# Optimization experiments

Measured on AMD Instinct MI355X. Metric: run time of the kernel, lower is better.

Reference implementation:

```python
import jax, jax.numpy as jnp
import numpy as np

N = 50000       # num nodes
F_IN = 256      # num_features
HID = 128       # num_hidden
E = 800000      # structural edges (no self loops)
E_KNN = 500000  # knn edges (no self loops)


def setup_inputs() -> dict:
    rng = np.random.default_rng(0)
    # loop-free random edges: col != row guaranteed
    row = rng.integers(0, N, E)
    col = (row + 1 + rng.integers(0, N - 1, E)) % N
    edge_index = jnp.asarray(np.stack([row, col]), dtype=jnp.int32)
    rowk = rng.integers(0, N, E_KNN)
    colk = (rowk + 1 + rng.integers(0, N - 1, E_KNN)) % N
    knn_graph = jnp.asarray(np.stack([rowk, colk]), dtype=jnp.int32)

    key = jax.random.key(0)
    ks = jax.random.split(key, 8)
    x = jax.random.normal(ks[0], (N, F_IN), dtype=jnp.float32)
    s = 1.0 / np.sqrt(F_IN)  # nn.Linear default init range
    def lin(kw, kb):
        W = jax.random.uniform(kw, (HID, F_IN), minval=-s, maxval=s, dtype=jnp.float32)
        b = jax.random.uniform(kb, (HID,), minval=-s, maxval=s, dtype=jnp.float32)
        return W, b
    W_s1, b_s1 = lin(ks[1], ks[2])
    W_s2, b_s2 = lin(ks[3], ks[4])
    W_f2, b_f2 = lin(ks[5], ks[6])
    return {"x": x, "edge_index": edge_index, "knn_graph": knn_graph,
            "W_s1": W_s1, "b_s1": b_s1, "W_s2": W_s2, "b_s2": b_s2,
            "W_f2": W_f2, "b_f2": b_f2}


def _gcn_norm(edge_index, num_nodes):
    # add_remaining_self_loops on loop-free input == append all self loops (w=1)
    loop = jnp.arange(num_nodes, dtype=edge_index.dtype)
    row = jnp.concatenate([edge_index[0], loop])
    col = jnp.concatenate([edge_index[1], loop])
    w = jnp.ones(row.shape[0], dtype=jnp.float32)
    deg = jax.ops.segment_sum(w, col, num_segments=num_nodes)
    dinv = jnp.where(deg > 0, jax.lax.rsqrt(deg), 0.0)
    return row, col, dinv[row] * w * dinv[col]


def _gcn(x, W, b, row, col, norm, K):
    # eval mode: dropout(p=0.6) is identity
    h = x @ W.T + b
    n = x.shape[0]
    for _ in range(K):
        # gather source feats -> edge-weight scale -> scatter-add to targets (SpMM)
        h = jax.ops.segment_sum(norm[:, None] * h[row], col, num_segments=n)
    return h


def reference(x, edge_index, knn_graph, W_s1, b_s1, W_s2, b_s2, W_f2, b_f2):
    n = x.shape[0]
    r, c, nm = _gcn_norm(edge_index, n)
    rk, ck, nmk = _gcn_norm(knn_graph, n)
    h0 = _gcn(x, W_s1, b_s1, r, c, nm, 2)
    h1 = _gcn(x, W_s2, b_s2, r, c, nm, 10)
    z0 = _gcn(x, W_f2, b_f2, r, c, nm, 2)
    # original computes gcn_f2(x, edge_index, K=2) twice; in eval mode both equal z0
    z1 = z0 + _gcn(x, W_f2, b_f2, rk, ck, nmk, 1)
    return (h0, h1, z0, z1)
```

## Files before the change

### kernel.cpp

```cpp
#include <hip/hip_runtime.h>
#include <hip/hip_fp16.h>

#define F_IN 256
#define HID 128

typedef _Float16 half8 __attribute__((ext_vector_type(8)));
typedef _Float16 half4v __attribute__((ext_vector_type(4)));
typedef float f32x4 __attribute__((ext_vector_type(4)));


__global__ void k_count(const int* __restrict__ col, int E, int* __restrict__ cnt) {
  int e = blockIdx.x * blockDim.x + threadIdx.x;
  if (e < E) atomicAdd(&cnt[col[e]], 1);
}

__global__ void k_scan_block(const int* __restrict__ in, int n, int* __restrict__ out,
                             int* __restrict__ bsum) {
  __shared__ int s[1024];
  int tid = threadIdx.x;
  int i = blockIdx.x * 1024 + tid;
  int v = (i < n) ? in[i] : 0;
  s[tid] = v;
  __syncthreads();
  for (int off = 1; off < 1024; off <<= 1) {
    int t = (tid >= off) ? s[tid - off] : 0;
    __syncthreads();
    s[tid] += t;
    __syncthreads();
  }
  if (i < n) out[i] = s[tid] - v;
  if (tid == 1023) bsum[blockIdx.x] = s[1023];
}

__global__ void k_scan_single(int* __restrict__ bsum, int nb, int* __restrict__ tail) {
  if (threadIdx.x == 0 && blockIdx.x == 0) {
    int run = 0;
    for (int b = 0; b < nb; ++b) { int t = bsum[b]; bsum[b] = run; run += t; }
    *tail = run;
  }
}

__global__ void k_add_off(int* __restrict__ out, const int* __restrict__ bsum, int n) {
  int i = blockIdx.x * blockDim.x + threadIdx.x;
  if (i < n) out[i] += bsum[i >> 10];
}

__global__ void k_scatter(const int* __restrict__ row, const int* __restrict__ col, int E,
                          const int* __restrict__ offs, int* __restrict__ cur,
                          int* __restrict__ csr) {
  int e = blockIdx.x * blockDim.x + threadIdx.x;
  if (e >= E) return;
  int c = col[e];
  int p = offs[c] + atomicAdd(&cur[c], 1);
  csr[p] = row[e];
}


__global__ void k_cvt_w(const float* __restrict__ W0, const float* __restrict__ W1,
                        const float* __restrict__ W2, _Float16* __restrict__ Wh) {
  const int sz = HID * F_IN;
  int idx = (blockIdx.x * 256 + threadIdx.x) * 4;
  const float* src = (idx < sz) ? (W0 + idx)
                   : (idx < 2 * sz) ? (W1 + idx - sz)
                   : (W2 + idx - 2 * sz);
  float4 v = *(const float4*)src;
  half4v o;
  o[0] = (_Float16)v.x; o[1] = (_Float16)v.y; o[2] = (_Float16)v.z; o[3] = (_Float16)v.w;
  *(half4v*)(Wh + idx) = o;
}


__global__ __launch_bounds__(256) void k_gemm3(
    const float* __restrict__ x, const _Float16* __restrict__ Wh,
    const float* __restrict__ b0, const float* __restrict__ b1, const float* __restrict__ b2,
    int n, const int* __restrict__ cnt_s, const int* __restrict__ cnt_k,
    _Float16* __restrict__ gS1, _Float16* __restrict__ gS2,
    _Float16* __restrict__ gF2s, _Float16* __restrict__ gF2k)
{
  int lane = threadIdx.x & 63;
  int wv = threadIdx.x >> 6;
  int l15 = lane & 15, lhi = lane >> 4;
  int mrow = blockIdx.x * 64 + wv * 16 + l15;
  bool mok = mrow < n;

  half8 a[8];
  {
    const float* xr = x + (size_t)mrow * F_IN;
#pragma unroll
    for (int kt = 0; kt < 8; ++kt) {
      float4 lo = make_float4(0.f, 0.f, 0.f, 0.f), hi = lo;
      if (mok) {
        lo = *(const float4*)(xr + kt * 32 + lhi * 8);
        hi = *(const float4*)(xr + kt * 32 + lhi * 8 + 4);
      }
      half8 v;
      v[0] = (_Float16)lo.x; v[1] = (_Float16)lo.y; v[2] = (_Float16)lo.z; v[3] = (_Float16)lo.w;
      v[4] = (_Float16)hi.x; v[5] = (_Float16)hi.y; v[6] = (_Float16)hi.z; v[7] = (_Float16)hi.w;
      a[kt] = v;
    }
  }

  float ss = 1.0f, sk = 1.0f;
  if (mok) {
    ss = rsqrtf((float)(cnt_s[mrow] + 1));
    sk = rsqrtf((float)(cnt_k[mrow] + 1));
  }

#pragma unroll
  for (int w = 0; w < 3; ++w) {
    const _Float16* Wp = Wh + (size_t)w * HID * F_IN;
    const float* bias = (w == 0) ? b0 : (w == 1) ? b1 : b2;
    _Float16* dst = (w == 0) ? gS1 : (w == 1) ? gS2 : gF2s;
    for (int nt = 0; nt < 8; ++nt) {
      const _Float16* wrow = Wp + (size_t)(nt * 16 + l15) * F_IN;
      int nbase = nt * 16 + lhi * 4;
      float4 bv = *(const float4*)(bias + nbase);
      f32x4 acc = {bv.x, bv.y, bv.z, bv.w};
#pragma unroll
      for (int kt = 0; kt < 8; ++kt) {
        half8 bf = *(const half8*)(wrow + kt * 32 + lhi * 8);
        acc = __builtin_amdgcn_mfma_f32_16x16x32_f16(bf, a[kt], acc, 0, 0, 0);
      }
      if (mok) {
        half4v o;
        o[0] = (_Float16)(acc[0] * ss); o[1] = (_Float16)(acc[1] * ss);
        o[2] = (_Float16)(acc[2] * ss); o[3] = (_Float16)(acc[3] * ss);
        *(half4v*)(dst + (size_t)mrow * HID + nbase) = o;
        if (w == 2) {
          half4v o2;
          o2[0] = (_Float16)(acc[0] * sk); o2[1] = (_Float16)(acc[1] * sk);
          o2[2] = (_Float16)(acc[2] * sk); o2[3] = (_Float16)(acc[3] * sk);
          *(half4v*)(gF2k + (size_t)mrow * HID + nbase) = o2;
        }
      }
    }
  }
}


__device__ inline float2 h2f2(unsigned int u) {
  __half2 h; *(unsigned int*)&h = u; return __half22float2(h);
}

__device__ inline void spmm_store(void* out, size_t base, float2 acc, float deg, int mode,
                                  const float2* __restrict__ add) {
  if (mode == 0) {
    float sc = 1.0f / deg;
    __half2 h = __float22half2_rn(make_float2(acc.x * sc, acc.y * sc));
    ((__half2*)out)[base] = h;
  } else {
    float sc = rsqrtf(deg);
    float2 o = make_float2(acc.x * sc, acc.y * sc);
    if (mode == 2) { float2 z = add[base]; o.x += z.x; o.y += z.y; }
    ((float2*)out)[base] = o;
  }
}

__global__ __launch_bounds__(256) void k_spmm_h(
    const unsigned int* __restrict__ gin, void* __restrict__ gout,
    const int* __restrict__ csr, const int* __restrict__ offs, const int* __restrict__ cnt,
    int n, int mode, const float2* __restrict__ addsrc)
{
  int w = (blockIdx.x << 2) | ((int)threadIdx.x >> 6);
  if (w >= n) return;
  int lane = threadIdx.x & 63;
  int beg = offs[w], end = offs[w + 1];
  size_t base = (size_t)w * 64 + lane;
  float2 acc = h2f2(gin[base]);
  int e = beg;
  for (; e + 4 <= end; e += 4) {
    unsigned int u0 = gin[(size_t)csr[e]     * 64 + lane];
    unsigned int u1 = gin[(size_t)csr[e + 1] * 64 + lane];
    unsigned int u2 = gin[(size_t)csr[e + 2] * 64 + lane];
    unsigned int u3 = gin[(size_t)csr[e + 3] * 64 + lane];
    float2 v0 = h2f2(u0), v1 = h2f2(u1), v2 = h2f2(u2), v3 = h2f2(u3);
    acc.x += v0.x + v1.x + v2.x + v3.x;
    acc.y += v0.y + v1.y + v2.y + v3.y;
  }
  for (; e < end; ++e) {
    float2 v = h2f2(gin[(size_t)csr[e] * 64 + lane]);
    acc.x += v.x; acc.y += v.y;
  }
  spmm_store(gout, base, acc, (float)(cnt[w] + 1), mode, addsrc);
}

__global__ __launch_bounds__(256) void k_spmm3(
    const unsigned int* __restrict__ g0, const unsigned int* __restrict__ g1,
    const unsigned int* __restrict__ g2,
    void* __restrict__ o0, void* __restrict__ o1, void* __restrict__ o2,
    int md0, int md1, int md2,
    const int* __restrict__ csr, const int* __restrict__ offs, const int* __restrict__ cnt,
    int n)
{
  int w = (blockIdx.x << 2) | ((int)threadIdx.x >> 6);
  if (w >= n) return;
  int lane = threadIdx.x & 63;
  int beg = offs[w], end = offs[w + 1];
  size_t base = (size_t)w * 64 + lane;
  float2 a0 = h2f2(g0[base]), a1 = h2f2(g1[base]), a2 = h2f2(g2[base]);
  int e = beg;
  for (; e + 2 <= end; e += 2) {
    size_t s0 = (size_t)csr[e] * 64 + lane;
    size_t s1 = (size_t)csr[e + 1] * 64 + lane;
    unsigned int u00 = g0[s0], u01 = g1[s0], u02 = g2[s0];
    unsigned int u10 = g0[s1], u11 = g1[s1], u12 = g2[s1];
    float2 v;
    v = h2f2(u00); a0.x += v.x; a0.y += v.y;
    v = h2f2(u01); a1.x += v.x; a1.y += v.y;
    v = h2f2(u02); a2.x += v.x; a2.y += v.y;
    v = h2f2(u10); a0.x += v.x; a0.y += v.y;
    v = h2f2(u11); a1.x += v.x; a1.y += v.y;
    v = h2f2(u12); a2.x += v.x; a2.y += v.y;
  }
  for (; e < end; ++e) {
    size_t s0 = (size_t)csr[e] * 64 + lane;
    float2 v;
    v = h2f2(g0[s0]); a0.x += v.x; a0.y += v.y;
    v = h2f2(g1[s0]); a1.x += v.x; a1.y += v.y;
    v = h2f2(g2[s0]); a2.x += v.x; a2.y += v.y;
  }
  float deg = (float)(cnt[w] + 1);
  spmm_store(o0, base, a0, deg, md0, nullptr);
  spmm_store(o1, base, a1, deg, md1, nullptr);
  spmm_store(o2, base, a2, deg, md2, nullptr);
}


extern "C" void kernel_launch(void* const* d_in, const int* in_sizes, int n_in,
                              void* d_out, int out_size, void* d_ws, size_t ws_size,
                              hipStream_t stream) {
  const float* x    = (const float*)d_in[0];
  const int*   ei   = (const int*)d_in[1];
  const int*   knn  = (const int*)d_in[2];
  const float* W_s1 = (const float*)d_in[3];
  const float* b_s1 = (const float*)d_in[4];
  const float* W_s2 = (const float*)d_in[5];
  const float* b_s2 = (const float*)d_in[6];
  const float* W_f2 = (const float*)d_in[7];
  const float* b_f2 = (const float*)d_in[8];

  const int N  = in_sizes[0] / F_IN;
  const int E  = in_sizes[1] / 2;
  const int EK = in_sizes[2] / 2;
  const int* row_s = ei;   const int* col_s = ei + E;
  const int* row_k = knn;  const int* col_k = knn + EK;

  char* p = (char*)d_ws;
  auto carve = [&](size_t bytes) {
    char* r = p; p += (bytes + 511) & ~(size_t)511; return (void*)r;
  };
  int* cnt_s = (int*)carve((size_t)N * 4);
  int* cnt_k = (int*)carve((size_t)N * 4);
  int* cur_s = (int*)carve((size_t)N * 4);
  int* cur_k = (int*)carve((size_t)N * 4);
  char* zero_end = p;
  int* offs_s = (int*)carve((size_t)(N + 1) * 4);
  int* offs_k = (int*)carve((size_t)(N + 1) * 4);
  int* bsum   = (int*)carve(4096);
  int* csr_s  = (int*)carve((size_t)E * 4);
  int* csr_k  = (int*)carve((size_t)EK * 4);
  _Float16* Wh  = (_Float16*)carve((size_t)3 * HID * F_IN * 2);
  _Float16* gS1 = (_Float16*)carve((size_t)N * HID * 2);
  _Float16* gS2 = (_Float16*)carve((size_t)N * HID * 2);
  _Float16* gF2s= (_Float16*)carve((size_t)N * HID * 2);
  _Float16* gF2k= (_Float16*)carve((size_t)N * HID * 2);
  _Float16* tS2 = (_Float16*)carve((size_t)N * HID * 2);

  float* out_h0 = (float*)d_out;
  float* out_h1 = out_h0 + (size_t)N * HID;
  float* out_z0 = out_h1 + (size_t)N * HID;
  float* out_z1 = out_z0 + (size_t)N * HID;
  _Float16* tS1 = (_Float16*)out_z1;
  _Float16* tF2 = tS1 + (size_t)N * HID;

  hipMemsetAsync(d_ws, 0, (size_t)(zero_end - (char*)d_ws), stream);

  const int tpb = 256;
  k_count<<<(E + tpb - 1) / tpb, tpb, 0, stream>>>(col_s, E, cnt_s);
  k_count<<<(EK + tpb - 1) / tpb, tpb, 0, stream>>>(col_k, EK, cnt_k);

  int nb = (N + 1023) / 1024;
  k_scan_block<<<nb, 1024, 0, stream>>>(cnt_s, N, offs_s, bsum);
  k_scan_single<<<1, 64, 0, stream>>>(bsum, nb, offs_s + N);
  k_add_off<<<(N + tpb - 1) / tpb, tpb, 0, stream>>>(offs_s, bsum, N);
  k_scan_block<<<nb, 1024, 0, stream>>>(cnt_k, N, offs_k, bsum);
  k_scan_single<<<1, 64, 0, stream>>>(bsum, nb, offs_k + N);
  k_add_off<<<(N + tpb - 1) / tpb, tpb, 0, stream>>>(offs_k, bsum, N);

  k_scatter<<<(E + tpb - 1) / tpb, tpb, 0, stream>>>(row_s, col_s, E, offs_s, cur_s, csr_s);
  k_scatter<<<(EK + tpb - 1) / tpb, tpb, 0, stream>>>(row_k, col_k, EK, offs_k, cur_k, csr_k);

  k_cvt_w<<<96, 256, 0, stream>>>(W_s1, W_s2, W_f2, Wh);
  k_gemm3<<<(N + 63) / 64, 256, 0, stream>>>(x, Wh, b_s1, b_s2, b_f2, N, cnt_s, cnt_k,
                                             gS1, gS2, gF2s, gF2k);

  int spmm_grid = (N + 3) / 4;

  k_spmm3<<<spmm_grid, 256, 0, stream>>>((const unsigned int*)gS1, (const unsigned int*)gS2,
                                         (const unsigned int*)gF2s,
                                         tS1, tS2, tF2, 0, 0, 0,
                                         csr_s, offs_s, cnt_s, N);
  k_spmm3<<<spmm_grid, 256, 0, stream>>>((const unsigned int*)tS1, (const unsigned int*)tS2,
                                         (const unsigned int*)tF2,
                                         out_h0, gS1, out_z0, 1, 0, 1,
                                         csr_s, offs_s, cnt_s, N);

  {
    _Float16* cur = gS1; _Float16* alt = tS2;
    for (int it = 0; it < 7; ++it) {
      k_spmm_h<<<spmm_grid, 256, 0, stream>>>((const unsigned int*)cur, alt,
                                              csr_s, offs_s, cnt_s, N, 0, nullptr);
      _Float16* t = cur; cur = alt; alt = t;
    }
    k_spmm_h<<<spmm_grid, 256, 0, stream>>>((const unsigned int*)cur, out_h1,
                                            csr_s, offs_s, cnt_s, N, 1, nullptr);
  }

  k_spmm_h<<<spmm_grid, 256, 0, stream>>>((const unsigned int*)gF2k, out_z1,
                                          csr_k, offs_k, cnt_k, N, 2,
                                          (const float2*)out_z0);
}
```

Before: 784.2 us.

## Merge count/scatter launches, split GEMM across weights, unroll SpMM gather by 8

Merges the structural and knn edge-count kernels into one launch, and does the same for the two CSR scatter kernels, to cut launch overhead. The three-weight GEMM now runs on a 2D grid with one weight matrix per blockIdx.y, which triples the number of blocks, adds an occupancy hint, and clamps out-of-range rows instead of branching. The cost is that each x tile is loaded three times. The single-feature SpMM loop is unrolled to 8 gathers plus a tail of 2, to put more loads in flight.

```diff
diff --git a/kernel.cpp b/kernel.cpp
--- a/kernel.cpp
+++ b/kernel.cpp
@@ -9,9 +9,15 @@
 typedef float f32x4 __attribute__((ext_vector_type(4)));
 
 
-__global__ void k_count(const int* __restrict__ col, int E, int* __restrict__ cnt) {
+__global__ void k_count2(const int* __restrict__ col_s, int E, int* __restrict__ cnt_s,
+                         const int* __restrict__ col_k, int EK, int* __restrict__ cnt_k) {
   int e = blockIdx.x * blockDim.x + threadIdx.x;
-  if (e < E) atomicAdd(&cnt[col[e]], 1);
+  if (e < E) {
+    atomicAdd(&cnt_s[col_s[e]], 1);
+  } else {
+    int f = e - E;
+    if (f < EK) atomicAdd(&cnt_k[col_k[f]], 1);
+  }
 }
 
 __global__ void k_scan_block(const int* __restrict__ in, int n, int* __restrict__ out,
@@ -45,14 +51,25 @@
   if (i < n) out[i] += bsum[i >> 10];
 }
 
-__global__ void k_scatter(const int* __restrict__ row, const int* __restrict__ col, int E,
-                          const int* __restrict__ offs, int* __restrict__ cur,
-                          int* __restrict__ csr) {
+__global__ void k_scatter2(const int* __restrict__ row_s, const int* __restrict__ col_s, int E,
+                           const int* __restrict__ offs_s, int* __restrict__ cur_s,
+                           int* __restrict__ csr_s,
+                           const int* __restrict__ row_k, const int* __restrict__ col_k, int EK,
+                           const int* __restrict__ offs_k, int* __restrict__ cur_k,
+                           int* __restrict__ csr_k) {
   int e = blockIdx.x * blockDim.x + threadIdx.x;
-  if (e >= E) return;
-  int c = col[e];
-  int p = offs[c] + atomicAdd(&cur[c], 1);
-  csr[p] = row[e];
+  if (e < E) {
+    int c = col_s[e];
+    int p = offs_s[c] + atomicAdd(&cur_s[c], 1);
+    csr_s[p] = row_s[e];
+  } else {
+    int f = e - E;
+    if (f < EK) {
+      int c = col_k[f];
+      int p = offs_k[c] + atomicAdd(&cur_k[c], 1);
+      csr_k[p] = row_k[f];
+    }
+  }
 }
 
 
@@ -70,68 +87,64 @@
 }
 
 
-__global__ __launch_bounds__(256) void k_gemm3(
+__global__ __launch_bounds__(256, 4) void k_gemm3(
     const float* __restrict__ x, const _Float16* __restrict__ Wh,
     const float* __restrict__ b0, const float* __restrict__ b1, const float* __restrict__ b2,
     int n, const int* __restrict__ cnt_s, const int* __restrict__ cnt_k,
     _Float16* __restrict__ gS1, _Float16* __restrict__ gS2,
     _Float16* __restrict__ gF2s, _Float16* __restrict__ gF2k)
 {
+  int w = blockIdx.y;
   int lane = threadIdx.x & 63;
   int wv = threadIdx.x >> 6;
   int l15 = lane & 15, lhi = lane >> 4;
   int mrow = blockIdx.x * 64 + wv * 16 + l15;
   bool mok = mrow < n;
+  int arow = mok ? mrow : (n - 1);
 
   half8 a[8];
   {
-    const float* xr = x + (size_t)mrow * F_IN;
+    const float* xr = x + (size_t)arow * F_IN;
 #pragma unroll
     for (int kt = 0; kt < 8; ++kt) {
-      float4 lo = make_float4(0.f, 0.f, 0.f, 0.f), hi = lo;
-      if (mok) {
-        lo = *(const float4*)(xr + kt * 32 + lhi * 8);
-        hi = *(const float4*)(xr + kt * 32 + lhi * 8 + 4);
-      }
+      float4 lo = *(const float4*)(xr + kt * 32 + lhi * 8);
+      float4 hi = *(const float4*)(xr + kt * 32 + lhi * 8 + 4);
       half8 v;
       v[0] = (_Float16)lo.x; v[1] = (_Float16)lo.y; v[2] = (_Float16)lo.z; v[3] = (_Float16)lo.w;
       v[4] = (_Float16)hi.x; v[5] = (_Float16)hi.y; v[6] = (_Float16)hi.z; v[7] = (_Float16)hi.w;
       a[kt] = v;
     }
   }
-
-  float ss = 1.0f, sk = 1.0f;
-  if (mok) {
-    ss = rsqrtf((float)(cnt_s[mrow] + 1));
-    sk = rsqrtf((float)(cnt_k[mrow] + 1));
-  }
-
 #pragma unroll
-  for (int w = 0; w < 3; ++w) {
-    const _Float16* Wp = Wh + (size_t)w * HID * F_IN;
-    const float* bias = (w == 0) ? b0 : (w == 1) ? b1 : b2;
-    _Float16* dst = (w == 0) ? gS1 : (w == 1) ? gS2 : gF2s;
-    for (int nt = 0; nt < 8; ++nt) {
-      const _Float16* wrow = Wp + (size_t)(nt * 16 + l15) * F_IN;
-      int nbase = nt * 16 + lhi * 4;
-      float4 bv = *(const float4*)(bias + nbase);
-      f32x4 acc = {bv.x, bv.y, bv.z, bv.w};
+  for (int kt = 0; kt < 8; ++kt) asm volatile("" :: "v"(a[kt]));
+
+  float ss = rsqrtf((float)(cnt_s[arow] + 1));
+  float sk = (w == 2) ? rsqrtf((float)(cnt_k[arow] + 1)) : 0.f;
+  const float* bias = (w == 0) ? b0 : (w == 1) ? b1 : b2;
+  _Float16* dst = (w == 0) ? gS1 : (w == 1) ? gS2 : gF2s;
+  const _Float16* Wp = Wh + (size_t)w * HID * F_IN;
+
 #pragma unroll
-      for (int kt = 0; kt < 8; ++kt) {
-        half8 bf = *(const half8*)(wrow + kt * 32 + lhi * 8);
-        acc = __builtin_amdgcn_mfma_f32_16x16x32_f16(bf, a[kt], acc, 0, 0, 0);
-      }
-      if (mok) {
-        half4v o;
-        o[0] = (_Float16)(acc[0] * ss); o[1] = (_Float16)(acc[1] * ss);
-        o[2] = (_Float16)(acc[2] * ss); o[3] = (_Float16)(acc[3] * ss);
-        *(half4v*)(dst + (size_t)mrow * HID + nbase) = o;
-        if (w == 2) {
-          half4v o2;
-          o2[0] = (_Float16)(acc[0] * sk); o2[1] = (_Float16)(acc[1] * sk);
-          o2[2] = (_Float16)(acc[2] * sk); o2[3] = (_Float16)(acc[3] * sk);
-          *(half4v*)(gF2k + (size_t)mrow * HID + nbase) = o2;
-        }
+  for (int nt = 0; nt < 8; ++nt) {
+    const _Float16* wrow = Wp + (size_t)(nt * 16 + l15) * F_IN;
+    int nbase = nt * 16 + lhi * 4;
+    float4 bv = *(const float4*)(bias + nbase);
+    f32x4 acc = {bv.x, bv.y, bv.z, bv.w};
+#pragma unroll
+    for (int kt = 0; kt < 8; ++kt) {
+      half8 bf = *(const half8*)(wrow + kt * 32 + lhi * 8);
+      acc = __builtin_amdgcn_mfma_f32_16x16x32_f16(bf, a[kt], acc, 0, 0, 0);
+    }
+    if (mok) {
+      half4v o;
+      o[0] = (_Float16)(acc[0] * ss); o[1] = (_Float16)(acc[1] * ss);
+      o[2] = (_Float16)(acc[2] * ss); o[3] = (_Float16)(acc[3] * ss);
+      *(half4v*)(dst + (size_t)mrow * HID + nbase) = o;
+      if (w == 2) {
+        half4v o2;
+        o2[0] = (_Float16)(acc[0] * sk); o2[1] = (_Float16)(acc[1] * sk);
+        o2[2] = (_Float16)(acc[2] * sk); o2[3] = (_Float16)(acc[3] * sk);
+        *(half4v*)(gF2k + (size_t)mrow * HID + nbase) = o2;
       }
     }
   }
@@ -168,16 +181,28 @@
   size_t base = (size_t)w * 64 + lane;
   float2 acc = h2f2(gin[base]);
   int e = beg;
-  for (; e + 4 <= end; e += 4) {
+  for (; e + 8 <= end; e += 8) {
     unsigned int u0 = gin[(size_t)csr[e]     * 64 + lane];
     unsigned int u1 = gin[(size_t)csr[e + 1] * 64 + lane];
     unsigned int u2 = gin[(size_t)csr[e + 2] * 64 + lane];
     unsigned int u3 = gin[(size_t)csr[e + 3] * 64 + lane];
+    unsigned int u4 = gin[(size_t)csr[e + 4] * 64 + lane];
+    unsigned int u5 = gin[(size_t)csr[e + 5] * 64 + lane];
+    unsigned int u6 = gin[(size_t)csr[e + 6] * 64 + lane];
+    unsigned int u7 = gin[(size_t)csr[e + 7] * 64 + lane];
     float2 v0 = h2f2(u0), v1 = h2f2(u1), v2 = h2f2(u2), v3 = h2f2(u3);
-    acc.x += v0.x + v1.x + v2.x + v3.x;
-    acc.y += v0.y + v1.y + v2.y + v3.y;
-  }
-  for (; e < end; ++e) {
+    float2 v4 = h2f2(u4), v5 = h2f2(u5), v6 = h2f2(u6), v7 = h2f2(u7);
+    acc.x += (v0.x + v1.x) + (v2.x + v3.x) + ((v4.x + v5.x) + (v6.x + v7.x));
+    acc.y += (v0.y + v1.y) + (v2.y + v3.y) + ((v4.y + v5.y) + (v6.y + v7.y));
+  }
+  for (; e + 2 <= end; e += 2) {
+    unsigned int u0 = gin[(size_t)csr[e]     * 64 + lane];
+    unsigned int u1 = gin[(size_t)csr[e + 1] * 64 + lane];
+    float2 v0 = h2f2(u0), v1 = h2f2(u1);
+    acc.x += v0.x + v1.x;
+    acc.y += v0.y + v1.y;
+  }
+  if (e < end) {
     float2 v = h2f2(gin[(size_t)csr[e] * 64 + lane]);
     acc.x += v.x; acc.y += v.y;
   }
@@ -276,8 +301,8 @@
   hipMemsetAsync(d_ws, 0, (size_t)(zero_end - (char*)d_ws), stream);
 
   const int tpb = 256;
-  k_count<<<(E + tpb - 1) / tpb, tpb, 0, stream>>>(col_s, E, cnt_s);
-  k_count<<<(EK + tpb - 1) / tpb, tpb, 0, stream>>>(col_k, EK, cnt_k);
+  int etot = E + EK;
+  k_count2<<<(etot + tpb - 1) / tpb, tpb, 0, stream>>>(col_s, E, cnt_s, col_k, EK, cnt_k);
 
   int nb = (N + 1023) / 1024;
   k_scan_block<<<nb, 1024, 0, stream>>>(cnt_s, N, offs_s, bsum);
@@ -287,12 +312,14 @@
   k_scan_single<<<1, 64, 0, stream>>>(bsum, nb, offs_k + N);
   k_add_off<<<(N + tpb - 1) / tpb, tpb, 0, stream>>>(offs_k, bsum, N);
 
-  k_scatter<<<(E + tpb - 1) / tpb, tpb, 0, stream>>>(row_s, col_s, E, offs_s, cur_s, csr_s);
-  k_scatter<<<(EK + tpb - 1) / tpb, tpb, 0, stream>>>(row_k, col_k, EK, offs_k, cur_k, csr_k);
+  k_scatter2<<<(etot + tpb - 1) / tpb, tpb, 0, stream>>>(
+      row_s, col_s, E, offs_s, cur_s, csr_s,
+      row_k, col_k, EK, offs_k, cur_k, csr_k);
 
   k_cvt_w<<<96, 256, 0, stream>>>(W_s1, W_s2, W_f2, Wh);
-  k_gemm3<<<(N + 63) / 64, 256, 0, stream>>>(x, Wh, b_s1, b_s2, b_f2, N, cnt_s, cnt_k,
-                                             gS1, gS2, gF2s, gF2k);
+  dim3 ggrid((N + 63) / 64, 3);
+  k_gemm3<<<ggrid, 256, 0, stream>>>(x, Wh, b_s1, b_s2, b_f2, N, cnt_s, cnt_k,
+                                     gS1, gS2, gF2s, gF2k);
 
   int spmm_grid = (N + 3) / 4;
 
```

New measurement: 737.0 us. -6.0%, faster.
